# Kernel tuning notes

Measured on AMD Instinct MI355X. Metric: run time of the kernel, lower is better.

Reference implementation:

```python
import jax, jax.numpy as jnp
import numpy as np

N_PRO = 100000
N_LIG = 100000
E = 500000
H = 128
CE = 18


def _lin_params(key, out_dim, in_dim, scale=0.02):
    kw, kb = jax.random.split(key)
    W = jax.random.normal(kw, (out_dim, in_dim), jnp.float32) * scale
    b = jax.random.normal(kb, (out_dim,), jnp.float32) * scale
    return W, b


def setup_inputs() -> dict:
    key = jax.random.key(0)
    ks = jax.random.split(key, 16)
    inp = {}
    inp['pro_x'] = jax.random.normal(ks[0], (N_PRO, H), jnp.float32)
    inp['lig_x'] = jax.random.normal(ks[1], (N_LIG, H), jnp.float32)
    pi = jax.random.randint(ks[2], (E,), 0, N_PRO)
    li = jax.random.randint(ks[3], (E,), 0, N_LIG)
    inp['cross_ei'] = jnp.stack([pi, li]).astype(jnp.int64)
    inp['cross_ea'] = jax.random.normal(ks[4], (E, CE), jnp.float32)
    inp['Wq_pro'], inp['bq_pro'] = _lin_params(ks[5], H, H)
    inp['Wk_lig'], inp['bk_lig'] = _lin_params(ks[6], H, H)
    inp['Wv_lig'], inp['bv_lig'] = _lin_params(ks[7], H, H)
    inp['Wq_lig'], inp['bq_lig'] = _lin_params(ks[8], H, H)
    inp['Wk_pro'], inp['bk_pro'] = _lin_params(ks[9], H, H)
    inp['Wv_pro'], inp['bv_pro'] = _lin_params(ks[10], H, H)
    inp['We_bias'] = jax.random.normal(ks[11], (CE,), jnp.float32) * 0.02  # Linear(CE,1,bias=False) weight
    inp['Wo_pro'], inp['bo_pro'] = _lin_params(ks[12], H, H)
    inp['Wo_lig'], inp['bo_lig'] = _lin_params(ks[13], H, H)
    inp['g_pro'] = jnp.ones((H,), jnp.float32)
    inp['be_pro'] = jnp.zeros((H,), jnp.float32)
    inp['g_lig'] = jnp.ones((H,), jnp.float32)
    inp['be_lig'] = jnp.zeros((H,), jnp.float32)
    return inp


def _layernorm(x, g, b, eps=1e-5):
    mu = jnp.mean(x, -1, keepdims=True)
    var = jnp.var(x, -1, keepdims=True)
    return (x - mu) * jax.lax.rsqrt(var + eps) * g + b


def _lin(x, W, b):
    return x @ W.T + b


def _attend(Q_src, K_tgt, V_tgt, bias, tgt_idx, n_tgt, scale):
    # per-edge score -> edge softmax over target nodes -> weighted scatter-add
    scores = jnp.sum(Q_src * K_tgt, -1) * scale + bias          # [E]
    scores = scores - jnp.max(scores)                            # global max, as in torch code
    exp_s = jnp.exp(scores)
    denom = jax.ops.segment_sum(exp_s, tgt_idx, num_segments=n_tgt)
    w = exp_s / (denom[tgt_idx] + 1e-8)                          # [E]
    return jax.ops.segment_sum(w[:, None] * V_tgt, tgt_idx, num_segments=n_tgt)  # [n_tgt, H]


def reference(pro_x, lig_x, cross_ei, cross_ea,
              Wq_pro, bq_pro, Wk_lig, bk_lig, Wv_lig, bv_lig,
              Wq_lig, bq_lig, Wk_pro, bk_pro, Wv_pro, bv_pro,
              We_bias, Wo_pro, bo_pro, Wo_lig, bo_lig,
              g_pro, be_pro, g_lig, be_lig):
    pi = cross_ei[0]
    li = cross_ei[1]
    h = pro_x.shape[1]
    scale = h ** (-0.5)
    bias = cross_ea @ We_bias                                    # [E]

    # protein <- ligand
    Qp = _lin(pro_x, Wq_pro, bq_pro)[pi]
    Kl = _lin(lig_x, Wk_lig, bk_lig)[li]
    Vl = _lin(lig_x, Wv_lig, bv_lig)[li]
    pro_upd = _attend(Qp, Kl, Vl, bias, pi, pro_x.shape[0], scale)
    pro_new = _layernorm(pro_x + _lin(pro_upd, Wo_pro, bo_pro), g_pro, be_pro)

    # ligand <- protein
    Ql = _lin(lig_x, Wq_lig, bq_lig)[li]
    Kp = _lin(pro_x, Wk_pro, bk_pro)[pi]
    Vp = _lin(pro_x, Wv_pro, bv_pro)[pi]
    lig_upd = _attend(Ql, Kp, Vp, bias, li, lig_x.shape[0], scale)
    lig_new = _layernorm(lig_x + _lin(lig_upd, Wo_lig, bo_lig), g_lig, be_lig)

    return (pro_new, lig_new)
```

## Files before the change

### kernel.cpp

```cpp
#include <hip/hip_runtime.h>
#include <float.h>
#include <math.h>


typedef __bf16 bf16x8 __attribute__((ext_vector_type(8)));
typedef float  f32x4  __attribute__((ext_vector_type(4)));
typedef float  f32x2  __attribute__((ext_vector_type(2)));
typedef unsigned int u32x2 __attribute__((ext_vector_type(2)));

__device__ __forceinline__ bf16x8 cvt8(const float* p) {
    f32x4 lo = *reinterpret_cast<const f32x4*>(p);
    f32x4 hi = *reinterpret_cast<const f32x4*>(p + 4);
    bf16x8 r;
    r[0] = (__bf16)lo[0]; r[1] = (__bf16)lo[1]; r[2] = (__bf16)lo[2]; r[3] = (__bf16)lo[3];
    r[4] = (__bf16)hi[0]; r[5] = (__bf16)hi[1]; r[6] = (__bf16)hi[2]; r[7] = (__bf16)hi[3];
    return r;
}

__device__ __forceinline__ u32x2 pack_fp8x8(const float* v) {
    int w0 = __builtin_amdgcn_cvt_pk_fp8_f32(v[0], v[1], 0, false);
    w0 = __builtin_amdgcn_cvt_pk_fp8_f32(v[2], v[3], w0, true);
    int w1 = __builtin_amdgcn_cvt_pk_fp8_f32(v[4], v[5], 0, false);
    w1 = __builtin_amdgcn_cvt_pk_fp8_f32(v[6], v[7], w1, true);
    u32x2 r; r[0] = (unsigned)w0; r[1] = (unsigned)w1;
    return r;
}

__device__ __forceinline__ void unpack_fp8x8(u32x2 p, float* out) {
    f32x2 t0 = __builtin_amdgcn_cvt_pk_f32_fp8((int)p[0], false);
    f32x2 t1 = __builtin_amdgcn_cvt_pk_f32_fp8((int)p[0], true);
    f32x2 t2 = __builtin_amdgcn_cvt_pk_f32_fp8((int)p[1], false);
    f32x2 t3 = __builtin_amdgcn_cvt_pk_f32_fp8((int)p[1], true);
    out[0] = t0[0]; out[1] = t0[1]; out[2] = t1[0]; out[3] = t1[1];
    out[4] = t2[0]; out[5] = t2[1]; out[6] = t3[0]; out[7] = t3[1];
}

__device__ __forceinline__ long pack_fp8x8_l(const float* v) {
    return __builtin_bit_cast(long, pack_fp8x8(v));
}

__device__ __forceinline__ void stage_w(const __bf16* __restrict__ Ws, char* wlds, int tid) {
#pragma unroll
    for (int it = 0; it < 8; ++it) {
        int idx = it * 2048 + tid * 8;
        int byteoff = idx * 2;
        int row = byteoff >> 8;
        *reinterpret_cast<bf16x8*>(wlds + (byteoff ^ ((row & 7) << 4)))
            = *reinterpret_cast<const bf16x8*>(Ws + idx);
    }
}
__device__ __forceinline__ bf16x8 read_w(const char* wlds, int l15, int lg, int ni, int ks) {
    int row = ni * 16 + l15;
    int off = (row * 256 + ks * 64 + lg * 16) ^ ((row & 7) << 4);
    return *reinterpret_cast<const bf16x8*>(wlds + off);
}

__device__ __forceinline__ void stage_w8(const unsigned char* __restrict__ W8m, char* dst, int tid) {
#pragma unroll
    for (int it = 0; it < 8; ++it) {
        int idx = it * 2048 + tid * 8;
        int row = idx >> 7, col = idx & 127;
        *reinterpret_cast<u32x2*>(dst + row * 136 + col)
            = *reinterpret_cast<const u32x2*>(W8m + idx);
    }
}
__device__ __forceinline__ long read_w8(const char* base, int l15, int lg, int ni, int ks) {
    int off = (ni * 16 + l15) * 136 + ks * 32 + lg * 8;
    return *reinterpret_cast<const long*>(base + off);
}

__global__ __launch_bounds__(256) void cvt_bias_count(
    const float* wq_p, const float* wk_p, const float* wv_p,
    const float* wq_l, const float* wk_l, const float* wv_l,
    const float* wo_p, const float* wo_l,
    unsigned char* __restrict__ W8, __bf16* __restrict__ W16,
    const float* __restrict__ ea, const float* __restrict__ We,
    const int* __restrict__ pi, const int* __restrict__ li,
    float* __restrict__ bias, int* __restrict__ counts,
    unsigned* __restrict__ ranks, int Np, int E, int CE)
{
    if (blockIdx.x < 48) {
        const float* srcs[6] = {wq_p, wk_p, wv_p, wq_l, wk_l, wv_l};
        int mat = blockIdx.x >> 3;
        int t = (blockIdx.x & 7) * 256 + threadIdx.x;
        int off = t * 8;
        float v[8];
        f32x4 lo = *reinterpret_cast<const f32x4*>(srcs[mat] + off);
        f32x4 hi = *reinterpret_cast<const f32x4*>(srcs[mat] + off + 4);
        v[0] = lo[0]; v[1] = lo[1]; v[2] = lo[2]; v[3] = lo[3];
        v[4] = hi[0]; v[5] = hi[1]; v[6] = hi[2]; v[7] = hi[3];
        *reinterpret_cast<u32x2*>(W8 + (size_t)mat * 16384 + off) = pack_fp8x8(v);
        return;
    }
    if (blockIdx.x < 64) {
        const float* srcs[2] = {wo_p, wo_l};
        int mat = (blockIdx.x - 48) >> 3;
        int t = ((blockIdx.x - 48) & 7) * 256 + threadIdx.x;
        int base = t * 8;
        const float* s = srcs[mat];
        __bf16* d = W16 + (size_t)mat * 16384;
#pragma unroll
        for (int u = 0; u < 8; ++u) {
            int idx = base + u;
            int row = idx >> 7, c = idx & 127;
            int pos = (c & 15) * 8 + (c >> 4);
            d[row * 128 + pos] = (__bf16)s[idx];
        }
        return;
    }
    int e = (blockIdx.x - 64) * 256 + threadIdx.x;
    if (e >= E) return;
    const float2* row = reinterpret_cast<const float2*>(ea + (size_t)e * CE);
    float acc = 0.f;
    int h = CE >> 1;
    for (int c = 0; c < h; ++c) {
        float2 v = row[c];
        acc += v.x * We[2 * c] + v.y * We[2 * c + 1];
    }
    if (CE & 1) acc += ea[(size_t)e * CE + CE - 1] * We[CE - 1];
    bias[e] = acc;
    int r0 = atomicAdd(&counts[pi[e]], 1);
    int r1 = atomicAdd(&counts[Np + li[e]], 1);
    ranks[e] = (unsigned)(r0 & 0xFFFF) | ((unsigned)r1 << 16);
}

__global__ __launch_bounds__(256) void scan1(
    const int* __restrict__ counts, int* __restrict__ offs,
    int* __restrict__ bsums, int N)
{
    int idx = blockIdx.x * 256 + threadIdx.x;
    int v = (idx < N) ? counts[idx] : 0;
    int lane = threadIdx.x & 63, w = threadIdx.x >> 6;
    int x = v;
#pragma unroll
    for (int d = 1; d < 64; d <<= 1) {
        int y = __shfl_up(x, d);
        if (lane >= d) x += y;
    }
    __shared__ int wsum[4];
    if (lane == 63) wsum[w] = x;
    __syncthreads();
    int add = 0;
    for (int i = 0; i < w; ++i) add += wsum[i];
    x += add;
    if (idx < N) offs[idx] = x - v;
    if (threadIdx.x == 255) bsums[blockIdx.x] = x;
}

__global__ __launch_bounds__(256) void scan3(
    int* __restrict__ offs, const int* __restrict__ bsums, int N, int total)
{
    int b = blockIdx.x, t = threadIdx.x;
    int s = 0;
    for (int i = t; i < b; i += 256) s += bsums[i];
#pragma unroll
    for (int d = 1; d < 64; d <<= 1) s += __shfl_xor(s, d);
    __shared__ int ws_[4];
    if ((t & 63) == 0) ws_[t >> 6] = s;
    __syncthreads();
    int pre = ws_[0] + ws_[1] + ws_[2] + ws_[3];
    int idx = b * 256 + t;
    if (idx < N) offs[idx] += pre;
    if (idx == 0) offs[N] = total;
}

__global__ __launch_bounds__(256) void fill2(
    const int* __restrict__ pi, const int* __restrict__ li,
    const float* __restrict__ bias, const unsigned* __restrict__ ranks,
    const int* __restrict__ offs, unsigned* __restrict__ elist, int Np, int E)
{
    int e = blockIdx.x * 256 + threadIdx.x;
    if (e >= E) return;
    int p = pi[e], l = li[e];
    unsigned rk = ranks[e];
    int w = __builtin_amdgcn_cvt_pk_fp8_f32(bias[e], 0.f, 0, false);
    unsigned b8 = (unsigned)w & 0xFFu;
    elist[offs[p] + (rk & 0xFFFFu)]  = ((unsigned)l << 8) | b8;
    elist[offs[Np + l] + (rk >> 16)] = ((unsigned)p << 8) | b8;
}

__global__ __launch_bounds__(256) void proj3both(
    const float* __restrict__ Xp, const float* __restrict__ Xl,
    const unsigned char* __restrict__ W8,
    const float* __restrict__ bq_p, const float* __restrict__ bk_p, const float* __restrict__ bv_p,
    const float* __restrict__ bq_l, const float* __restrict__ bk_l, const float* __restrict__ bv_l,
    char* __restrict__ QKVp, char* __restrict__ QKVl,
    int Np, int Nl, int nbp)
{
    __shared__ char wlds[52224];
    int bid = blockIdx.x;
    int tid = threadIdx.x;
    int lane = tid & 63, wv = tid >> 6;
    int l15 = lane & 15, lg = lane >> 4;

    const float* A; const unsigned char* Wb8;
    const float* bsels[3]; char* QKV; int M, wrow;
    if (bid < nbp) {
        A = Xp; M = Np; wrow = bid * 64 + wv * 16;
        Wb8 = W8;
        bsels[0] = bq_p; bsels[1] = bk_p; bsels[2] = bv_p; QKV = QKVp;
    } else {
        A = Xl; M = Nl; wrow = (bid - nbp) * 64 + wv * 16;
        Wb8 = W8 + 3 * 16384;
        bsels[0] = bq_l; bsels[1] = bk_l; bsels[2] = bv_l; QKV = QKVl;
    }

    stage_w8(Wb8 + 0 * 16384, wlds + 0 * 17408, tid);
    stage_w8(Wb8 + 1 * 16384, wlds + 1 * 17408, tid);
    stage_w8(Wb8 + 2 * 16384, wlds + 2 * 17408, tid);

    int r0 = wrow + l15; if (r0 > M - 1) r0 = M - 1;
    const float* Arow0 = A + (size_t)r0 * 128 + lg * 8;

    long a8[4];
#pragma unroll
    for (int ks = 0; ks < 4; ++ks) {
        float v[8];
        f32x4 lo = *reinterpret_cast<const f32x4*>(Arow0 + ks * 32);
        f32x4 hi = *reinterpret_cast<const f32x4*>(Arow0 + ks * 32 + 4);
        v[0] = lo[0]; v[1] = lo[1]; v[2] = lo[2]; v[3] = lo[3];
        v[4] = hi[0]; v[5] = hi[1]; v[6] = hi[2]; v[7] = hi[3];
        a8[ks] = pack_fp8x8_l(v);
    }
    __syncthreads();

#pragma unroll
    for (int mat = 0; mat < 3; ++mat) {
        const char* wl = wlds + mat * 17408;
        f32x4 acc[8] = {};
#pragma unroll
        for (int ks = 0; ks < 4; ++ks) {
#pragma unroll
            for (int ni = 0; ni < 8; ++ni)
                acc[ni] = __builtin_amdgcn_mfma_f32_16x16x32_fp8_fp8(
                    a8[ks], read_w8(wl, l15, lg, ni, ks), acc[ni], 0, 0, 0);
        }
        float bc[8];
#pragma unroll
        for (int ni = 0; ni < 8; ++ni) bc[ni] = bsels[mat][ni * 16 + l15];
#pragma unroll
        for (int r = 0; r < 4; ++r) {
            int row = wrow + lg * 4 + r;
            if (row < M) {
                float v[8];
#pragma unroll
                for (int ni = 0; ni < 8; ++ni) v[ni] = acc[ni][r] + bc[ni];
                char* rowb = QKV + (size_t)row * 512;
                if (mat == 0) {
                    bf16x8 o;
#pragma unroll
                    for (int ni = 0; ni < 8; ++ni) o[ni] = (__bf16)v[ni];
                    *reinterpret_cast<bf16x8*>(rowb + l15 * 16) = o;
                } else {
                    *reinterpret_cast<u32x2*>(rowb + 256 + (mat - 1) * 128 + l15 * 8)
                        = pack_fp8x8(v);
                }
            }
        }
    }
}

__global__ __launch_bounds__(256) void attend(
    const char* __restrict__ QKVp, const char* __restrict__ QKVl,
    const unsigned* __restrict__ elist, const int* __restrict__ offs,
    __bf16* __restrict__ upd_pro, __bf16* __restrict__ upd_lig,
    int Np, int Ntot, float scale)
{
    int node = blockIdx.x * 16 + (threadIdx.x >> 4);
    if (node >= Ntot) return;
    int l = threadIdx.x & 15;
    const char* Qrow; const char* KV; __bf16* upd;
    if (node < Np) {
        Qrow = QKVp + (size_t)node * 512; KV = QKVl;
        upd = upd_pro + (size_t)node * 128;
    } else {
        int n = node - Np;
        Qrow = QKVl + (size_t)n * 512; KV = QKVp;
        upd = upd_lig + (size_t)n * 128;
    }
    bf16x8 qv = *reinterpret_cast<const bf16x8*>(Qrow + l * 16);
    float q[8];
#pragma unroll
    for (int j = 0; j < 8; ++j) q[j] = (float)qv[j];

    int beg = offs[node], end = offs[node + 1];
    float d = 0.f;
    float acc[8] = {};
    int i = beg;
    for (; i + 1 < end; i += 2) {
        unsigned rec0 = elist[i], rec1 = elist[i + 1];
        const char* row0 = KV + (size_t)(rec0 >> 8) * 512;
        const char* row1 = KV + (size_t)(rec1 >> 8) * 512;
        u32x2 kk0 = *reinterpret_cast<const u32x2*>(row0 + 256 + l * 8);
        u32x2 vp0 = *reinterpret_cast<const u32x2*>(row0 + 384 + l * 8);
        u32x2 kk1 = *reinterpret_cast<const u32x2*>(row1 + 256 + l * 8);
        u32x2 vp1 = *reinterpret_cast<const u32x2*>(row1 + 384 + l * 8);
        float kf0[8], vf0[8], kf1[8], vf1[8];
        unpack_fp8x8(kk0, kf0); unpack_fp8x8(vp0, vf0);
        unpack_fp8x8(kk1, kf1); unpack_fp8x8(vp1, vf1);
        float dot0 = 0.f, dot1 = 0.f;
#pragma unroll
        for (int j = 0; j < 8; ++j) { dot0 += q[j] * kf0[j]; dot1 += q[j] * kf1[j]; }
#pragma unroll
        for (int t = 1; t < 16; t <<= 1) {
            dot0 += __shfl_xor(dot0, t, 16);
            dot1 += __shfl_xor(dot1, t, 16);
        }
        f32x2 b0 = __builtin_amdgcn_cvt_pk_f32_fp8((int)(rec0 & 0xFFu), false);
        f32x2 b1 = __builtin_amdgcn_cvt_pk_f32_fp8((int)(rec1 & 0xFFu), false);
        float p0 = __expf(fminf(dot0 * scale + b0[0], 60.f));
        float p1 = __expf(fminf(dot1 * scale + b1[0], 60.f));
        d += p0 + p1;
#pragma unroll
        for (int j = 0; j < 8; ++j) acc[j] += p0 * vf0[j] + p1 * vf1[j];
    }
    if (i < end) {
        unsigned rec = elist[i];
        const char* row = KV + (size_t)(rec >> 8) * 512;
        u32x2 kk = *reinterpret_cast<const u32x2*>(row + 256 + l * 8);
        u32x2 vp = *reinterpret_cast<const u32x2*>(row + 384 + l * 8);
        float kf[8], vf[8];
        unpack_fp8x8(kk, kf); unpack_fp8x8(vp, vf);
        float dot = 0.f;
#pragma unroll
        for (int j = 0; j < 8; ++j) dot += q[j] * kf[j];
#pragma unroll
        for (int t = 1; t < 16; t <<= 1) dot += __shfl_xor(dot, t, 16);
        f32x2 bt = __builtin_amdgcn_cvt_pk_f32_fp8((int)(rec & 0xFFu), false);
        float p = __expf(fminf(dot * scale + bt[0], 60.f));
        d += p;
#pragma unroll
        for (int j = 0; j < 8; ++j) acc[j] += p * vf[j];
    }
    float inv = 1.f / (d + 1e-8f);
    bf16x8 o;
#pragma unroll
    for (int j = 0; j < 8; ++j) o[j] = (__bf16)(acc[j] * inv);
    *reinterpret_cast<bf16x8*>(upd + l * 8) = o;
}

__global__ __launch_bounds__(256) void gemm_ln_both(
    const __bf16* __restrict__ upd_pro, const __bf16* __restrict__ upd_lig,
    const float* __restrict__ Xp, const float* __restrict__ Xl,
    const __bf16* __restrict__ W16,
    const float* __restrict__ bo_p, const float* __restrict__ g_p, const float* __restrict__ be_p,
    const float* __restrict__ bo_l, const float* __restrict__ g_l, const float* __restrict__ be_l,
    float* __restrict__ out_pro, float* __restrict__ out_lig,
    int Np, int Nl, int nbp)
{
    __shared__ char wlds[32768];
    int bid = blockIdx.x;
    int tid = threadIdx.x;
    int lane = tid & 63, wv = tid >> 6;
    int l15 = lane & 15, lg = lane >> 4;

    const __bf16* A; const float* X; const __bf16* Wo;
    const float *b, *g, *be_; float* C; int M, wrow;
    if (bid < nbp) {
        A = upd_pro; X = Xp; Wo = W16;
        b = bo_p; g = g_p; be_ = be_p; C = out_pro; M = Np; wrow = bid * 64 + wv * 16;
    } else {
        A = upd_lig; X = Xl; Wo = W16 + 16384;
        b = bo_l; g = g_l; be_ = be_l; C = out_lig; M = Nl; wrow = (bid - nbp) * 64 + wv * 16;
    }
    stage_w(Wo, wlds, tid);

    int r0 = wrow + l15; if (r0 > M - 1) r0 = M - 1;
    const __bf16* Arow0 = A + (size_t)r0 * 128 + lg * 8;
    bf16x8 a0[4];
#pragma unroll
    for (int ks = 0; ks < 4; ++ks)
        a0[ks] = *reinterpret_cast<const bf16x8*>(Arow0 + ks * 32);
    __syncthreads();

    f32x4 acc[8] = {};
#pragma unroll
    for (int ks = 0; ks < 4; ++ks) {
#pragma unroll
        for (int ni = 0; ni < 8; ++ni)
            acc[ni] = __builtin_amdgcn_mfma_f32_16x16x32_bf16(
                a0[ks], read_w(wlds, l15, lg, ni, ks), acc[ni], 0, 0, 0);
    }

    float bcol[8], gcol[8], becol[8];
#pragma unroll
    for (int ni = 0; ni < 8; ++ni) {
        bcol[ni]  = b[ni * 16 + l15];
        gcol[ni]  = g[ni * 16 + l15];
        becol[ni] = be_[ni * 16 + l15];
    }

#pragma unroll
    for (int r = 0; r < 4; ++r) {
        int row = wrow + lg * 4 + r;
        bool ok = row < M;
        int rowc = ok ? row : M - 1;
        float v[8];
#pragma unroll
        for (int ni = 0; ni < 8; ++ni) v[ni] = acc[ni][r] + bcol[ni];
        const float* Xr = X + (size_t)rowc * 128 + l15;
        float s1 = 0.f, s2 = 0.f;
#pragma unroll
        for (int ni = 0; ni < 8; ++ni) {
            v[ni] += Xr[ni * 16];
            s1 += v[ni]; s2 += v[ni] * v[ni];
        }
#pragma unroll
        for (int d = 1; d < 16; d <<= 1) {
            s1 += __shfl_xor(s1, d);
            s2 += __shfl_xor(s2, d);
        }
        float mu = s1 * 0.0078125f;
        float var = s2 * 0.0078125f - mu * mu;
        float rstd = rsqrtf(var + 1e-5f);
        if (ok) {
            float* Cr = C + (size_t)row * 128 + l15;
#pragma unroll
            for (int ni = 0; ni < 8; ++ni)
                Cr[ni * 16] = (v[ni] - mu) * rstd * gcol[ni] + becol[ni];
        }
    }
}

static inline int cdiv(int a, int b) { return (a + b - 1) / b; }

extern "C" void kernel_launch(void* const* d_in, const int* in_sizes, int n_in,
                              void* d_out, int out_size, void* d_ws, size_t ws_size,
                              hipStream_t stream)
{
    const float* pro_x  = (const float*)d_in[0];
    const float* lig_x  = (const float*)d_in[1];
    const int*   ei     = (const int*)d_in[2];
    const float* ea     = (const float*)d_in[3];
    const float* Wq_pro = (const float*)d_in[4];  const float* bq_pro = (const float*)d_in[5];
    const float* Wk_lig = (const float*)d_in[6];  const float* bk_lig = (const float*)d_in[7];
    const float* Wv_lig = (const float*)d_in[8];  const float* bv_lig = (const float*)d_in[9];
    const float* Wq_lig = (const float*)d_in[10]; const float* bq_lig = (const float*)d_in[11];
    const float* Wk_pro = (const float*)d_in[12]; const float* bk_pro = (const float*)d_in[13];
    const float* Wv_pro = (const float*)d_in[14]; const float* bv_pro = (const float*)d_in[15];
    const float* We     = (const float*)d_in[16];
    const float* Wo_pro = (const float*)d_in[17]; const float* bo_pro = (const float*)d_in[18];
    const float* Wo_lig = (const float*)d_in[19]; const float* bo_lig = (const float*)d_in[20];
    const float* g_pro  = (const float*)d_in[21]; const float* be_pro = (const float*)d_in[22];
    const float* g_lig  = (const float*)d_in[23]; const float* be_lig = (const float*)d_in[24];

    const int Np = in_sizes[0] / 128;
    const int Nl = in_sizes[1] / 128;
    const int E  = in_sizes[2] / 2;
    const int CE = in_sizes[3] / E;
    const int Nmax = Np > Nl ? Np : Nl;
    const int Ntot = Np + Nl;
    const int* pi = ei;
    const int* li = ei + E;

    float* out_pro = (float*)d_out;
    float* out_lig = out_pro + (size_t)Np * 128;

    float* ws = (float*)d_ws;
    size_t o = 0;
    char* QKVp = (char*)(ws + o); o += (size_t)Nmax * 128;
    char* QKVl = (char*)(ws + o); o += (size_t)Nmax * 128;
    float* bias = ws + o;   o += (size_t)E;
    unsigned* ranks = (unsigned*)(ws + o); o += (size_t)E;
    unsigned* elist = (unsigned*)(ws + o); o += 2 * (size_t)E;
    int* counts = (int*)(ws + o); o += (size_t)Ntot + 8;
    int* offs   = (int*)(ws + o); o += (size_t)Ntot + 8;
    int* bsums  = (int*)(ws + o); o += 4096;
    unsigned char* W8 = (unsigned char*)(ws + o); o += 6 * 16384 / 4;
    __bf16* W16 = (__bf16*)(ws + o); o += 2 * 16384 / 2;
    __bf16* upd = (__bf16*)(ws + o); o += (size_t)Ntot * 64;
    __bf16* upd_pro = upd;
    __bf16* upd_lig = upd + (size_t)Np * 128;
    (void)ws_size; (void)n_in; (void)out_size;

    const float scale = 1.0f / sqrtf(128.0f);
    const int nEB = cdiv(E, 256);

    (void)hipMemsetAsync(counts, 0, (size_t)(Ntot + 8) * sizeof(int), stream);
    cvt_bias_count<<<64 + nEB, 256, 0, stream>>>(
        Wq_pro, Wk_pro, Wv_pro, Wq_lig, Wk_lig, Wv_lig, Wo_pro, Wo_lig,
        W8, W16, ea, We, pi, li, bias, counts, ranks, Np, E, CE);

    const int nb1 = cdiv(Ntot, 256);
    scan1<<<nb1, 256, 0, stream>>>(counts, offs, bsums, Ntot);
    scan3<<<nb1, 256, 0, stream>>>(offs, bsums, Ntot, 2 * E);
    fill2<<<nEB, 256, 0, stream>>>(pi, li, bias, ranks, offs, elist, Np, E);

    const int nbp = cdiv(Np, 64), nbl = cdiv(Nl, 64);
    proj3both<<<nbp + nbl, 256, 0, stream>>>(pro_x, lig_x, W8,
        bq_pro, bk_pro, bv_pro, bq_lig, bk_lig, bv_lig,
        QKVp, QKVl, Np, Nl, nbp);

    attend<<<cdiv(Ntot, 16), 256, 0, stream>>>(QKVp, QKVl, elist, offs,
        upd_pro, upd_lig, Np, Ntot, scale);

    gemm_ln_both<<<nbp + nbl, 256, 0, stream>>>(upd_pro, upd_lig,
        pro_x, lig_x, W16, bo_pro, g_pro, be_pro, bo_lig, g_lig, be_lig,
        out_pro, out_lig, Np, Nl, nbp);
}
```

Before: 242.2 us.

## Merge edge-list fill into projection kernel and batch 4 edges per thread in counting

```diff
diff --git a/kernel.cpp b/kernel.cpp
--- a/kernel.cpp
+++ b/kernel.cpp
@@ -7,15 +7,6 @@
 typedef float  f32x4  __attribute__((ext_vector_type(4)));
 typedef float  f32x2  __attribute__((ext_vector_type(2)));
 typedef unsigned int u32x2 __attribute__((ext_vector_type(2)));
-
-__device__ __forceinline__ bf16x8 cvt8(const float* p) {
-    f32x4 lo = *reinterpret_cast<const f32x4*>(p);
-    f32x4 hi = *reinterpret_cast<const f32x4*>(p + 4);
-    bf16x8 r;
-    r[0] = (__bf16)lo[0]; r[1] = (__bf16)lo[1]; r[2] = (__bf16)lo[2]; r[3] = (__bf16)lo[3];
-    r[4] = (__bf16)hi[0]; r[5] = (__bf16)hi[1]; r[6] = (__bf16)hi[2]; r[7] = (__bf16)hi[3];
-    return r;
-}
 
 __device__ __forceinline__ u32x2 pack_fp8x8(const float* v) {
     int w0 = __builtin_amdgcn_cvt_pk_fp8_f32(v[0], v[1], 0, false);
@@ -108,20 +99,41 @@
         }
         return;
     }
-    int e = (blockIdx.x - 64) * 256 + threadIdx.x;
-    if (e >= E) return;
-    const float2* row = reinterpret_cast<const float2*>(ea + (size_t)e * CE);
-    float acc = 0.f;
-    int h = CE >> 1;
-    for (int c = 0; c < h; ++c) {
-        float2 v = row[c];
-        acc += v.x * We[2 * c] + v.y * We[2 * c + 1];
-    }
-    if (CE & 1) acc += ea[(size_t)e * CE + CE - 1] * We[CE - 1];
-    bias[e] = acc;
-    int r0 = atomicAdd(&counts[pi[e]], 1);
-    int r1 = atomicAdd(&counts[Np + li[e]], 1);
-    ranks[e] = (unsigned)(r0 & 0xFFFF) | ((unsigned)r1 << 16);
+    int ebase = (blockIdx.x - 64) * 1024 + threadIdx.x;
+    int ev[4]; int pv[4], lv[4]; float bv[4]; int r0v[4], r1v[4]; bool ok[4];
+#pragma unroll
+    for (int u = 0; u < 4; ++u) {
+        int e = ebase + u * 256;
+        ev[u] = e; ok[u] = e < E;
+        if (ok[u]) { pv[u] = pi[e]; lv[u] = li[e]; }
+    }
+#pragma unroll
+    for (int u = 0; u < 4; ++u) {
+        if (ok[u]) {
+            const float2* row = reinterpret_cast<const float2*>(ea + (size_t)ev[u] * CE);
+            float acc = 0.f;
+            int h = CE >> 1;
+            for (int c = 0; c < h; ++c) {
+                float2 v = row[c];
+                acc += v.x * We[2 * c] + v.y * We[2 * c + 1];
+            }
+            if (CE & 1) acc += ea[(size_t)ev[u] * CE + CE - 1] * We[CE - 1];
+            bv[u] = acc;
+        }
+    }
+#pragma unroll
+    for (int u = 0; u < 4; ++u)
+        if (ok[u]) r0v[u] = atomicAdd(&counts[pv[u]], 1);
+#pragma unroll
+    for (int u = 0; u < 4; ++u)
+        if (ok[u]) r1v[u] = atomicAdd(&counts[Np + lv[u]], 1);
+#pragma unroll
+    for (int u = 0; u < 4; ++u) {
+        if (ok[u]) {
+            bias[ev[u]] = bv[u];
+            ranks[ev[u]] = (unsigned)(r0v[u] & 0xFFFF) | ((unsigned)r1v[u] << 16);
+        }
+    }
 }
 
 __global__ __launch_bounds__(256) void scan1(
@@ -164,32 +176,33 @@
     if (idx == 0) offs[N] = total;
 }
 
-__global__ __launch_bounds__(256) void fill2(
-    const int* __restrict__ pi, const int* __restrict__ li,
-    const float* __restrict__ bias, const unsigned* __restrict__ ranks,
-    const int* __restrict__ offs, unsigned* __restrict__ elist, int Np, int E)
-{
-    int e = blockIdx.x * 256 + threadIdx.x;
-    if (e >= E) return;
-    int p = pi[e], l = li[e];
-    unsigned rk = ranks[e];
-    int w = __builtin_amdgcn_cvt_pk_fp8_f32(bias[e], 0.f, 0, false);
-    unsigned b8 = (unsigned)w & 0xFFu;
-    elist[offs[p] + (rk & 0xFFFFu)]  = ((unsigned)l << 8) | b8;
-    elist[offs[Np + l] + (rk >> 16)] = ((unsigned)p << 8) | b8;
-}
-
-__global__ __launch_bounds__(256) void proj3both(
+__global__ __launch_bounds__(256) void proj_fill(
     const float* __restrict__ Xp, const float* __restrict__ Xl,
     const unsigned char* __restrict__ W8,
     const float* __restrict__ bq_p, const float* __restrict__ bk_p, const float* __restrict__ bv_p,
     const float* __restrict__ bq_l, const float* __restrict__ bk_l, const float* __restrict__ bv_l,
     char* __restrict__ QKVp, char* __restrict__ QKVl,
-    int Np, int Nl, int nbp)
+    const int* __restrict__ pi, const int* __restrict__ li,
+    const float* __restrict__ bias, const unsigned* __restrict__ ranks,
+    const int* __restrict__ offs, unsigned* __restrict__ elist,
+    int Np, int Nl, int nbp, int nbProj, int E)
 {
     __shared__ char wlds[52224];
     int bid = blockIdx.x;
     int tid = threadIdx.x;
+
+    if (bid >= nbProj) {
+        int e = (bid - nbProj) * 256 + tid;
+        if (e >= E) return;
+        int p = pi[e], l = li[e];
+        unsigned rk = ranks[e];
+        int w = __builtin_amdgcn_cvt_pk_fp8_f32(bias[e], 0.f, 0, false);
+        unsigned b8 = (unsigned)w & 0xFFu;
+        elist[offs[p] + (rk & 0xFFFFu)]  = ((unsigned)l << 8) | b8;
+        elist[offs[Np + l] + (rk >> 16)] = ((unsigned)p << 8) | b8;
+        return;
+    }
+
     int lane = tid & 63, wv = tid >> 6;
     int l15 = lane & 15, lg = lane >> 4;
 
@@ -475,21 +488,23 @@
 
     const float scale = 1.0f / sqrtf(128.0f);
     const int nEB = cdiv(E, 256);
+    const int nEB4 = cdiv(E, 1024);
 
     (void)hipMemsetAsync(counts, 0, (size_t)(Ntot + 8) * sizeof(int), stream);
-    cvt_bias_count<<<64 + nEB, 256, 0, stream>>>(
+    cvt_bias_count<<<64 + nEB4, 256, 0, stream>>>(
         Wq_pro, Wk_pro, Wv_pro, Wq_lig, Wk_lig, Wv_lig, Wo_pro, Wo_lig,
         W8, W16, ea, We, pi, li, bias, counts, ranks, Np, E, CE);
 
     const int nb1 = cdiv(Ntot, 256);
     scan1<<<nb1, 256, 0, stream>>>(counts, offs, bsums, Ntot);
     scan3<<<nb1, 256, 0, stream>>>(offs, bsums, Ntot, 2 * E);
-    fill2<<<nEB, 256, 0, stream>>>(pi, li, bias, ranks, offs, elist, Np, E);
 
     const int nbp = cdiv(Np, 64), nbl = cdiv(Nl, 64);
-    proj3both<<<nbp + nbl, 256, 0, stream>>>(pro_x, lig_x, W8,
+    const int nbProj = nbp + nbl;
+    proj_fill<<<nbProj + nEB, 256, 0, stream>>>(pro_x, lig_x, W8,
         bq_pro, bk_pro, bv_pro, bq_lig, bk_lig, bv_lig,
-        QKVp, QKVl, Np, Nl, nbp);
+        QKVp, QKVl, pi, li, bias, ranks, offs, elist,
+        Np, Nl, nbp, nbProj, E);
 
     attend<<<cdiv(Ntot, 16), 256, 0, stream>>>(QKVp, QKVl, elist, offs,
         upd_pro, upd_lig, Np, Ntot, scale);
```

Result: faster. 231.4 us (-4.4%).
